# Optimization experiments

Measured on AMD Instinct MI355X. Metric: run time of the kernel, lower is better.

Reference implementation:

```python
import jax, jax.numpy as jnp
import numpy as np

T_CH = 512
C_CH = 512
RED = 16
K = int(T_CH * 0.3)  # 153


def setup_inputs() -> dict:
    key = jax.random.key(0)
    ks = jax.random.split(key, 12)
    h_t, h_c = T_CH // RED, C_CH // RED
    s = 0.05
    return {
        "x_t": jax.random.normal(ks[0], (16, T_CH, 64, 64), jnp.float32),
        "x_c": jax.random.normal(ks[1], (16, C_CH, 64, 64), jnp.float32),
        # SE branch t: Linear(T,T/r) -> ReLU -> Linear(T/r,T) -> Sigmoid (weights stored as (in,out))
        "w1_t": jax.random.normal(ks[2], (T_CH, h_t), jnp.float32) * s,
        "b1_t": jnp.zeros((h_t,), jnp.float32),
        "w2_t": jax.random.normal(ks[3], (h_t, T_CH), jnp.float32) * s,
        "b2_t": jnp.zeros((T_CH,), jnp.float32),
        # SE branch c
        "w1_c": jax.random.normal(ks[4], (C_CH, h_c), jnp.float32) * s,
        "b1_c": jnp.zeros((h_c,), jnp.float32),
        "w2_c": jax.random.normal(ks[5], (h_c, C_CH), jnp.float32) * s,
        "b2_c": jnp.zeros((C_CH,), jnp.float32),
        # cross-channel attention parameter, shape (t_channels, c_channels)
        "cross_att": jax.random.normal(ks[6], (T_CH, C_CH), jnp.float32),
    }


def reference(x_t, x_c, w1_t, b1_t, w2_t, b2_t, w1_c, b1_c, w2_c, b2_c, cross_att):
    ct = x_t.shape[1]
    # AdaptiveAvgPool2d(1) -> global mean over spatial, then SE MLP + sigmoid
    att_t = jnp.mean(x_t, axis=(2, 3))                      # [b, ct]
    att_t = jax.nn.sigmoid(jax.nn.relu(att_t @ w1_t + b1_t) @ w2_t + b2_t)
    att_c = jnp.mean(x_c, axis=(2, 3))                      # [b, cc]
    att_c = jax.nn.sigmoid(jax.nn.relu(att_c @ w1_c + b1_c) @ w2_c + b2_c)

    # top-k hard mask over t-channels (scatter of constant 1.0)
    _, topk_idx = jax.lax.top_k(att_t, K)                   # [b, K]
    sparse_att_t = jax.nn.one_hot(topk_idx, ct, dtype=att_t.dtype).sum(axis=1)  # [b, ct]

    cross_w = jax.nn.softmax(cross_att, axis=-1)            # [ct, cc]

    # einsum('bt,tc,bchw->bthw'): GEMM over channels then broadcast mask
    cross_t = sparse_att_t[:, :, None, None] * jnp.einsum('tc,bchw->bthw', cross_w, x_c)
    # einsum('bc,tc,bthw->bchw') with cross_w.T labeled 'tc' => sum_t cross_w[c,t] * x_t
    cross_c = att_c[:, :, None, None] * jnp.einsum('ct,bthw->bchw', cross_w, x_t)

    out_t = x_t * att_t[:, :, None, None] + cross_t
    out_c = x_c * att_c[:, :, None, None] + cross_c
    return out_t, out_c
```

## Files before the change

kernel.cpp:

```cpp
#include <hip/hip_runtime.h>

#define NBATCH 16
#define CH 512
#define HID 32
#define KTOP 153
#define SP 4096
#define NELEM (NBATCH*CH*SP)

typedef __bf16 bf16x8 __attribute__((ext_vector_type(8)));
typedef float f32x16 __attribute__((ext_vector_type(16)));

__device__ __forceinline__ unsigned short f2bf(float f) {
    union { float f; unsigned u; } v; v.f = f;
    unsigned r = v.u + 0x7FFFu + ((v.u >> 16) & 1u);
    return (unsigned short)(r >> 16);
}

__global__ __launch_bounds__(256) void k1_reduce_transpose(
    const float* __restrict__ xt, const float* __restrict__ xc,
    unsigned short* __restrict__ xbt, unsigned short* __restrict__ xbc,
    float* __restrict__ psum)
{
    int sb = blockIdx.x, chb = blockIdx.y, bz = blockIdx.z;
    int b = bz >> 1, br = bz & 1;
    const float* x = br ? xc : xt;
    unsigned short* xb = br ? xbc : xbt;
    int t = threadIdx.x, lane = t & 63, w = t >> 6;
    int s0 = sb * 64, ch0 = chb * 64;

    __shared__ float G[64 * 73];

    const float* xbase = x + (size_t)b * CH * SP + s0 + lane;
    #pragma unroll
    for (int it = 0; it < 4; ++it)
        #pragma unroll
        for (int i = 0; i < 4; ++i) {
            int chl = w * 4 + i + 16 * it;
            G[chl * 73 + lane] = xbase[(size_t)(ch0 + chl) * SP];
        }
    __syncthreads();

    {
        int chl = t & 63, q = t >> 6;
        const float* row = &G[chl * 73 + q * 16];
        float s = 0.f;
        #pragma unroll
        for (int i = 0; i < 16; ++i) s += row[i];
        G[chl * 73 + 64 + q] = s;
    }
    __syncthreads();

    if (t < 64) {
        const float* p = &G[t * 73 + 64];
        float s = p[0] + p[1] + p[2] + p[3];
        psum[((size_t)sb * 32 + (br * 16 + b)) * CH + ch0 + t] = s;
    }

    size_t orow = (size_t)b * SP + s0;
    #pragma unroll
    for (int q = 0; q < 4; ++q) {
        int gid = q * 256 + t;
        int sl = gid >> 4;
        int c4 = (gid & 15) * 4;
        ushort4 d;
        d.x = f2bf(G[(c4 + 0) * 73 + sl]);
        d.y = f2bf(G[(c4 + 1) * 73 + sl]);
        d.z = f2bf(G[(c4 + 2) * 73 + sl]);
        d.w = f2bf(G[(c4 + 3) * 73 + sl]);
        *(ushort4*)&xb[(orow + sl) * CH + ch0 + c4] = d;
    }
}

__global__ __launch_bounds__(512) void k2_se(
    const float* __restrict__ psum,
    const float* __restrict__ w1t, const float* __restrict__ b1t,
    const float* __restrict__ w2t, const float* __restrict__ b2t,
    const float* __restrict__ w1c, const float* __restrict__ b1c,
    const float* __restrict__ w2c, const float* __restrict__ b2c,
    float* __restrict__ sAt, float* __restrict__ sBt, float* __restrict__ attc)
{
    int b = blockIdx.x, br = blockIdx.y;
    int bb = br * 16 + b;
    int t = threadIdx.x;
    __shared__ float satt[512];
    __shared__ float ph[16][33];
    __shared__ float sh[32];
    __shared__ float sval[512];

    float s = 0.f;
    #pragma unroll
    for (int j = 0; j < 64; ++j) s += psum[((size_t)j * 32 + bb) * CH + t];
    satt[t] = s * (1.0f / 4096.0f);
    __syncthreads();

    const float* w1 = br ? w1c : w1t; const float* b1 = br ? b1c : b1t;
    const float* w2 = br ? w2c : w2t; const float* b2 = br ? b2c : b2t;

    {
        int j = t & 31, seg = t >> 5;
        float hp = 0.f;
        #pragma unroll
        for (int i = 0; i < 32; ++i)
            hp += satt[seg * 32 + i] * w1[(seg * 32 + i) * HID + j];
        ph[seg][j] = hp;
    }
    __syncthreads();
    if (t < HID) {
        float h = b1[t];
        #pragma unroll
        for (int sgi = 0; sgi < 16; ++sgi) h += ph[sgi][t];
        sh[t] = fmaxf(h, 0.0f);
    }
    __syncthreads();

    float z = b2[t];
    #pragma unroll
    for (int j = 0; j < HID; ++j) z += sh[j] * w2[j * CH + t];
    float a = 1.0f / (1.0f + expf(-z));

    if (br == 0) {
        sval[t] = a;
        __syncthreads();
        int cnt = 0;
        for (int j = 0; j < CH; ++j) {
            float o = sval[j];
            cnt += (o > a) || (o == a && j < t);
        }
        sAt[b * CH + t] = a;
        sBt[b * CH + t] = (cnt < KTOP) ? 1.0f : 0.0f;
    } else {
        attc[b * CH + t] = a;
    }
}

__global__ __launch_bounds__(64) void k2_softmax(
    const float* __restrict__ ca, unsigned short* __restrict__ wswz)
{
    int trow = blockIdx.x;
    int lane = threadIdx.x;
    const float* row = ca + (size_t)trow * CH;
    float v[8];
    #pragma unroll
    for (int i = 0; i < 8; ++i) v[i] = row[lane * 8 + i];
    float m = v[0];
    #pragma unroll
    for (int i = 1; i < 8; ++i) m = fmaxf(m, v[i]);
    #pragma unroll
    for (int off = 32; off; off >>= 1) m = fmaxf(m, __shfl_xor(m, off, 64));
    float s = 0.f;
    #pragma unroll
    for (int i = 0; i < 8; ++i) { v[i] = expf(v[i] - m); s += v[i]; }
    #pragma unroll
    for (int off = 32; off; off >>= 1) s += __shfl_xor(s, off, 64);
    float inv = 1.0f / s;

    int k = lane * 8;
    int kb = k >> 5, ks = (k >> 4) & 1, hi = (k >> 3) & 1;
    int p = ((kb * 16 + (trow >> 5)) * 2 + ks) * 64 + hi * 32 + (trow & 31);
    unsigned short* dst = wswz + (size_t)p * 8;
    ushort4 lo, hm;
    lo.x = f2bf(v[0] * inv); lo.y = f2bf(v[1] * inv);
    lo.z = f2bf(v[2] * inv); lo.w = f2bf(v[3] * inv);
    hm.x = f2bf(v[4] * inv); hm.y = f2bf(v[5] * inv);
    hm.z = f2bf(v[6] * inv); hm.w = f2bf(v[7] * inv);
    *(ushort4*)dst = lo;
    *(ushort4*)(dst + 4) = hm;
}

__global__ __launch_bounds__(256, 2) void k3_gemm(
    const unsigned short* __restrict__ xbt, const unsigned short* __restrict__ xbc,
    const unsigned short* __restrict__ wswz,
    const float* __restrict__ xt, const float* __restrict__ xc,
    const float* __restrict__ sAt, const float* __restrict__ sBt,
    const float* __restrict__ attc,
    float* __restrict__ out)
{
    int nt = blockIdx.x, b = blockIdx.y, g = blockIdx.z;
    int t = threadIdx.x, lane = t & 63, w = t >> 6;
    int n0 = nt * 64;

    const unsigned short* xb = g ? xbt : xbc;
    const float* xref = g ? xc : xt;
    const float* sA = g ? attc : sAt;
    const float* sB = g ? attc : sBt;

    f32x16 acc[4][2];
    #pragma unroll
    for (int r = 0; r < 4; ++r)
        #pragma unroll
        for (int c = 0; c < 2; ++c)
            #pragma unroll
            for (int e = 0; e < 16; ++e) acc[r][c][e] = 0.0f;

    const unsigned short* abase = wswz + ((size_t)(w * 4 * 2 * 64 + lane)) * 8;
    const unsigned short* bbase = xb + ((size_t)b * SP + n0 + (lane & 31)) * CH
                                     + (lane >> 5) * 8;

    bf16x8 afr[2][8], bfr[2][4];

    #pragma unroll
    for (int r = 0; r < 4; ++r)
        #pragma unroll
        for (int ks = 0; ks < 2; ++ks)
            afr[0][r * 2 + ks] = *(const bf16x8*)(abase + r * 1024 + ks * 512);
    #pragma unroll
    for (int c = 0; c < 2; ++c)
        #pragma unroll
        for (int ks = 0; ks < 2; ++ks)
            bfr[0][c * 2 + ks] = *(const bf16x8*)(bbase + c * 16384 + ks * 16);

    #pragma unroll
    for (int kb = 0; kb < 16; ++kb) {
        int cur = kb & 1, nxt = cur ^ 1;
        if (kb < 15) {
            #pragma unroll
            for (int r = 0; r < 4; ++r)
                #pragma unroll
                for (int ks = 0; ks < 2; ++ks)
                    afr[nxt][r * 2 + ks] =
                        *(const bf16x8*)(abase + (kb + 1) * 16384 + r * 1024 + ks * 512);
            #pragma unroll
            for (int c = 0; c < 2; ++c)
                #pragma unroll
                for (int ks = 0; ks < 2; ++ks)
                    bfr[nxt][c * 2 + ks] =
                        *(const bf16x8*)(bbase + c * 16384 + (kb + 1) * 32 + ks * 16);
        }
        #pragma unroll
        for (int ks = 0; ks < 2; ++ks)
            #pragma unroll
            for (int r = 0; r < 4; ++r)
                #pragma unroll
                for (int c = 0; c < 2; ++c)
                    acc[r][c] = __builtin_amdgcn_mfma_f32_32x32x16_bf16(
                        afr[cur][r * 2 + ks], bfr[cur][c * 2 + ks], acc[r][c], 0, 0, 0);
    }

    size_t outg = (size_t)g * NELEM;
    int colbase = n0 + (lane & 31);
    int rowq = 4 * (lane >> 5);
    #pragma unroll
    for (int r = 0; r < 4; ++r) {
        #pragma unroll
        for (int reg = 0; reg < 16; ++reg) {
            int m = w * 128 + r * 32 + (reg & 3) + 8 * (reg >> 2) + rowq;
            float sav = sA[b * CH + m];
            float sbv = sB[b * CH + m];
            #pragma unroll
            for (int c = 0; c < 2; ++c) {
                size_t idx = ((size_t)b * CH + m) * SP + colbase + c * 32;
                out[outg + idx] = sav * xref[idx] + sbv * acc[r][c][reg];
            }
        }
    }
}

extern "C" void kernel_launch(void* const* d_in, const int* in_sizes, int n_in,
                              void* d_out, int out_size, void* d_ws, size_t ws_size,
                              hipStream_t stream)
{
    const float* xt  = (const float*)d_in[0];
    const float* xc  = (const float*)d_in[1];
    const float* w1t = (const float*)d_in[2];
    const float* b1t = (const float*)d_in[3];
    const float* w2t = (const float*)d_in[4];
    const float* b2t = (const float*)d_in[5];
    const float* w1c = (const float*)d_in[6];
    const float* b1c = (const float*)d_in[7];
    const float* w2c = (const float*)d_in[8];
    const float* b2c = (const float*)d_in[9];
    const float* ca  = (const float*)d_in[10];
    float* out = (float*)d_out;
    char* ws = (char*)d_ws;

    unsigned short* xbt  = (unsigned short*)(ws);
    unsigned short* xbc  = (unsigned short*)(ws + 67108864ull);
    unsigned short* wswz = (unsigned short*)(ws + 134217728ull);
    float* psum = (float*)(ws + 134742016ull);
    float* sAt  = (float*)(ws + 138936320ull);
    float* sBt  = (float*)(ws + 138969088ull);
    float* attc = (float*)(ws + 139001856ull);

    hipLaunchKernelGGL(k1_reduce_transpose, dim3(64, 8, 32), dim3(256), 0, stream,
                       xt, xc, xbt, xbc, psum);
    hipLaunchKernelGGL(k2_se, dim3(16, 2), dim3(512), 0, stream,
                       psum, w1t, b1t, w2t, b2t, w1c, b1c, w2c, b2c, sAt, sBt, attc);
    hipLaunchKernelGGL(k2_softmax, dim3(512), dim3(64), 0, stream, ca, wswz);
    hipLaunchKernelGGL(k3_gemm, dim3(64, 16, 2), dim3(256), 0, stream,
                       xbt, xbc, wswz, xt, xc, sAt, sBt, attc, out);
}
```

Before: 713.3 us.

## Fuse bf16 transpose into GEMM via LDS staging, drop transposed workspace

The first kernel now only computes per-channel spatial sums with vectorized loads and wave shuffles, so it no longer writes bf16 transposed copies of both inputs to global memory. The GEMM kernel loads a 32-column fp32 tile of both x_t and x_c for one batch, converts it to bf16 and stores it in swizzled shared memory. It then computes both cross products from that tile, so each A fragment is reused for two outputs. Output stores become nontemporal. This removes a large global write and re-read of intermediate data, at the cost of 64 KB of LDS per block, lower occupancy, and narrower N tiles.

```diff
diff --git a/kernel.cpp b/kernel.cpp
--- a/kernel.cpp
+++ b/kernel.cpp
@@ -16,59 +16,25 @@
     return (unsigned short)(r >> 16);
 }
 
-__global__ __launch_bounds__(256) void k1_reduce_transpose(
+__global__ __launch_bounds__(256) void k1_reduce(
     const float* __restrict__ xt, const float* __restrict__ xc,
-    unsigned short* __restrict__ xbt, unsigned short* __restrict__ xbc,
     float* __restrict__ psum)
 {
-    int sb = blockIdx.x, chb = blockIdx.y, bz = blockIdx.z;
+    int c4 = blockIdx.x, bz = blockIdx.y;
     int b = bz >> 1, br = bz & 1;
     const float* x = br ? xc : xt;
-    unsigned short* xb = br ? xbc : xbt;
     int t = threadIdx.x, lane = t & 63, w = t >> 6;
-    int s0 = sb * 64, ch0 = chb * 64;
-
-    __shared__ float G[64 * 73];
-
-    const float* xbase = x + (size_t)b * CH * SP + s0 + lane;
-    #pragma unroll
-    for (int it = 0; it < 4; ++it)
-        #pragma unroll
-        for (int i = 0; i < 4; ++i) {
-            int chl = w * 4 + i + 16 * it;
-            G[chl * 73 + lane] = xbase[(size_t)(ch0 + chl) * SP];
-        }
-    __syncthreads();
-
-    {
-        int chl = t & 63, q = t >> 6;
-        const float* row = &G[chl * 73 + q * 16];
-        float s = 0.f;
-        #pragma unroll
-        for (int i = 0; i < 16; ++i) s += row[i];
-        G[chl * 73 + 64 + q] = s;
-    }
-    __syncthreads();
-
-    if (t < 64) {
-        const float* p = &G[t * 73 + 64];
-        float s = p[0] + p[1] + p[2] + p[3];
-        psum[((size_t)sb * 32 + (br * 16 + b)) * CH + ch0 + t] = s;
-    }
-
-    size_t orow = (size_t)b * SP + s0;
-    #pragma unroll
-    for (int q = 0; q < 4; ++q) {
-        int gid = q * 256 + t;
-        int sl = gid >> 4;
-        int c4 = (gid & 15) * 4;
-        ushort4 d;
-        d.x = f2bf(G[(c4 + 0) * 73 + sl]);
-        d.y = f2bf(G[(c4 + 1) * 73 + sl]);
-        d.z = f2bf(G[(c4 + 2) * 73 + sl]);
-        d.w = f2bf(G[(c4 + 3) * 73 + sl]);
-        *(ushort4*)&xb[(orow + sl) * CH + ch0 + c4] = d;
-    }
+    int ch = c4 * 4 + w;
+    const float4* p = (const float4*)(x + ((size_t)b * CH + ch) * SP);
+    float s = 0.f;
+    #pragma unroll
+    for (int k = 0; k < 16; ++k) {
+        float4 v = p[lane + k * 64];
+        s += ((v.x + v.y) + (v.z + v.w));
+    }
+    #pragma unroll
+    for (int off = 32; off; off >>= 1) s += __shfl_xor(s, off, 64);
+    if (lane == 0) psum[(size_t)(br * 16 + b) * CH + ch] = s;
 }
 
 __global__ __launch_bounds__(512) void k2_se(
@@ -87,10 +53,7 @@
     __shared__ float sh[32];
     __shared__ float sval[512];
 
-    float s = 0.f;
-    #pragma unroll
-    for (int j = 0; j < 64; ++j) s += psum[((size_t)j * 32 + bb) * CH + t];
-    satt[t] = s * (1.0f / 4096.0f);
+    satt[t] = psum[(size_t)bb * CH + t] * (1.0f / 4096.0f);
     __syncthreads();
 
     const float* w1 = br ? w1c : w1t; const float* b1 = br ? b1c : b1t;
@@ -167,36 +130,64 @@
     *(ushort4*)(dst + 4) = hm;
 }
 
-__global__ __launch_bounds__(256, 2) void k3_gemm(
-    const unsigned short* __restrict__ xbt, const unsigned short* __restrict__ xbc,
+__global__ __launch_bounds__(256, 2) void k3_fused(
+    const float* __restrict__ xt, const float* __restrict__ xc,
     const unsigned short* __restrict__ wswz,
-    const float* __restrict__ xt, const float* __restrict__ xc,
     const float* __restrict__ sAt, const float* __restrict__ sBt,
     const float* __restrict__ attc,
     float* __restrict__ out)
 {
-    int nt = blockIdx.x, b = blockIdx.y, g = blockIdx.z;
+    int nt = blockIdx.x, b = blockIdx.y;
     int t = threadIdx.x, lane = t & 63, w = t >> 6;
-    int n0 = nt * 64;
-
-    const unsigned short* xb = g ? xbt : xbc;
-    const float* xref = g ? xc : xt;
-    const float* sA = g ? attc : sAt;
-    const float* sB = g ? attc : sBt;
-
-    f32x16 acc[4][2];
+    int n0 = nt * 32;
+
+    __shared__ unsigned short B2[2][32 * 512];
+
+    {
+        int a  = t & 7;
+        int cq = t >> 3;
+        #pragma unroll
+        for (int src = 0; src < 2; ++src) {
+            const float* x = src ? xc : xt;
+            char* bl = (char*)B2[src];
+            const float* gbase = x + (size_t)b * CH * SP + n0 + a * 4;
+            #pragma unroll
+            for (int chb = 0; chb < 4; ++chb) {
+                int q = chb * 32 + cq;
+                float4 v0 = *(const float4*)(gbase + (size_t)(q * 4 + 0) * SP);
+                float4 v1 = *(const float4*)(gbase + (size_t)(q * 4 + 1) * SP);
+                float4 v2 = *(const float4*)(gbase + (size_t)(q * 4 + 2) * SP);
+                float4 v3 = *(const float4*)(gbase + (size_t)(q * 4 + 3) * SP);
+                #pragma unroll
+                for (int j = 0; j < 4; ++j) {
+                    int n = a * 4 + j;
+                    ushort4 d;
+                    d.x = f2bf(((const float*)&v0)[j]);
+                    d.y = f2bf(((const float*)&v1)[j]);
+                    d.z = f2bf(((const float*)&v2)[j]);
+                    d.w = f2bf(((const float*)&v3)[j]);
+                    int bo = n * 1024 + ((q * 8) ^ ((n & 7) << 4));
+                    *(ushort4*)(bl + bo) = d;
+                }
+            }
+        }
+    }
+    __syncthreads();
+
+    f32x16 acct[4], accc[4];
     #pragma unroll
     for (int r = 0; r < 4; ++r)
         #pragma unroll
-        for (int c = 0; c < 2; ++c)
-            #pragma unroll
-            for (int e = 0; e < 16; ++e) acc[r][c][e] = 0.0f;
+        for (int e = 0; e < 16; ++e) { acct[r][e] = 0.0f; accc[r][e] = 0.0f; }
 
     const unsigned short* abase = wswz + ((size_t)(w * 4 * 2 * 64 + lane)) * 8;
-    const unsigned short* bbase = xb + ((size_t)b * SP + n0 + (lane & 31)) * CH
-                                     + (lane >> 5) * 8;
-
-    bf16x8 afr[2][8], bfr[2][4];
+    const char* btl = (const char*)B2[0];
+    const char* bcl = (const char*)B2[1];
+    int nb = (lane & 31) * 1024;
+    int xr = (lane & 7) << 4;
+    int kf = (lane >> 5) * 16;
+
+    bf16x8 afr[2][8], bft[2][2], bfc[2][2];
 
     #pragma unroll
     for (int r = 0; r < 4; ++r)
@@ -204,10 +195,11 @@
         for (int ks = 0; ks < 2; ++ks)
             afr[0][r * 2 + ks] = *(const bf16x8*)(abase + r * 1024 + ks * 512);
     #pragma unroll
-    for (int c = 0; c < 2; ++c)
-        #pragma unroll
-        for (int ks = 0; ks < 2; ++ks)
-            bfr[0][c * 2 + ks] = *(const bf16x8*)(bbase + c * 16384 + ks * 16);
+    for (int ks = 0; ks < 2; ++ks) {
+        int off = nb + ((ks * 32 + kf) ^ xr);
+        bft[0][ks] = *(const bf16x8*)(btl + off);
+        bfc[0][ks] = *(const bf16x8*)(bcl + off);
+    }
 
     #pragma unroll
     for (int kb = 0; kb < 16; ++kb) {
@@ -220,37 +212,38 @@
                     afr[nxt][r * 2 + ks] =
                         *(const bf16x8*)(abase + (kb + 1) * 16384 + r * 1024 + ks * 512);
             #pragma unroll
-            for (int c = 0; c < 2; ++c)
-                #pragma unroll
-                for (int ks = 0; ks < 2; ++ks)
-                    bfr[nxt][c * 2 + ks] =
-                        *(const bf16x8*)(bbase + c * 16384 + (kb + 1) * 32 + ks * 16);
+            for (int ks = 0; ks < 2; ++ks) {
+                int off = nb + ((((kb + 1) * 64) + ks * 32 + kf) ^ xr);
+                bft[nxt][ks] = *(const bf16x8*)(btl + off);
+                bfc[nxt][ks] = *(const bf16x8*)(bcl + off);
+            }
         }
         #pragma unroll
         for (int ks = 0; ks < 2; ++ks)
             #pragma unroll
-            for (int r = 0; r < 4; ++r)
-                #pragma unroll
-                for (int c = 0; c < 2; ++c)
-                    acc[r][c] = __builtin_amdgcn_mfma_f32_32x32x16_bf16(
-                        afr[cur][r * 2 + ks], bfr[cur][c * 2 + ks], acc[r][c], 0, 0, 0);
-    }
-
-    size_t outg = (size_t)g * NELEM;
-    int colbase = n0 + (lane & 31);
+            for (int r = 0; r < 4; ++r) {
+                acct[r] = __builtin_amdgcn_mfma_f32_32x32x16_bf16(
+                    afr[cur][r * 2 + ks], bfc[cur][ks], acct[r], 0, 0, 0);
+                accc[r] = __builtin_amdgcn_mfma_f32_32x32x16_bf16(
+                    afr[cur][r * 2 + ks], bft[cur][ks], accc[r], 0, 0, 0);
+            }
+    }
+
+    int colb = n0 + (lane & 31);
     int rowq = 4 * (lane >> 5);
     #pragma unroll
     for (int r = 0; r < 4; ++r) {
         #pragma unroll
         for (int reg = 0; reg < 16; ++reg) {
             int m = w * 128 + r * 32 + (reg & 3) + 8 * (reg >> 2) + rowq;
-            float sav = sA[b * CH + m];
-            float sbv = sB[b * CH + m];
-            #pragma unroll
-            for (int c = 0; c < 2; ++c) {
-                size_t idx = ((size_t)b * CH + m) * SP + colbase + c * 32;
-                out[outg + idx] = sav * xref[idx] + sbv * acc[r][c][reg];
-            }
+            size_t idx = ((size_t)b * CH + m) * SP + colb;
+            float at = sAt[b * CH + m];
+            float bt = sBt[b * CH + m];
+            float ac = attc[b * CH + m];
+            float ot = at * xt[idx] + bt * acct[r][reg];
+            float oc = ac * xc[idx] + ac * accc[r][reg];
+            __builtin_nontemporal_store(ot, &out[idx]);
+            __builtin_nontemporal_store(oc, &out[NELEM + idx]);
         }
     }
 }
@@ -273,19 +266,17 @@
     float* out = (float*)d_out;
     char* ws = (char*)d_ws;
 
-    unsigned short* xbt  = (unsigned short*)(ws);
-    unsigned short* xbc  = (unsigned short*)(ws + 67108864ull);
-    unsigned short* wswz = (unsigned short*)(ws + 134217728ull);
-    float* psum = (float*)(ws + 134742016ull);
-    float* sAt  = (float*)(ws + 138936320ull);
-    float* sBt  = (float*)(ws + 138969088ull);
-    float* attc = (float*)(ws + 139001856ull);
-
-    hipLaunchKernelGGL(k1_reduce_transpose, dim3(64, 8, 32), dim3(256), 0, stream,
-                       xt, xc, xbt, xbc, psum);
+    unsigned short* wswz = (unsigned short*)(ws);
+    float* psum = (float*)(ws + 524288ull);
+    float* sAt  = (float*)(ws + 589824ull);
+    float* sBt  = (float*)(ws + 622592ull);
+    float* attc = (float*)(ws + 655360ull);
+
+    hipLaunchKernelGGL(k1_reduce, dim3(128, 32), dim3(256), 0, stream,
+                       xt, xc, psum);
     hipLaunchKernelGGL(k2_se, dim3(16, 2), dim3(512), 0, stream,
                        psum, w1t, b1t, w2t, b2t, w1c, b1c, w2c, b2c, sAt, sBt, attc);
     hipLaunchKernelGGL(k2_softmax, dim3(512), dim3(64), 0, stream, ca, wswz);
-    hipLaunchKernelGGL(k3_gemm, dim3(64, 16, 2), dim3(256), 0, stream,
-                       xbt, xbc, wswz, xt, xc, sAt, sBt, attc, out);
-}
+    hipLaunchKernelGGL(k3_fused, dim3(128, 16), dim3(256), 0, stream,
+                       xt, xc, wswz, sAt, sBt, attc, out);
+}
```

Result: faster. 671.5 us (-5.9%).
